# Kernel tuning notes

Measured on AMD Instinct MI355X. Metric: run time of the kernel, lower is better.

Reference implementation:

```python
import jax, jax.numpy as jnp
import numpy as np

N_EVENT = 100000
N_TRACE = 20000
E_EE = 1000000
E_ET = 500000
E_TE = 500000
D = 128          # embedding_dim == hidden_dim
OUT = 64         # output_dim
L = 3            # num_layers
NTYPES_EDGES = 3 # edge types
B = 64           # graphs per batch


def setup_inputs() -> dict:
    key = jax.random.key(0)
    ks = jax.random.split(key, 16)
    s = 1.0 / np.sqrt(D)
    inp = {
        "event_ids": jnp.arange(N_EVENT, dtype=jnp.int64 if jax.config.jax_enable_x64 else jnp.int32),
        "trace_ids": jnp.arange(N_TRACE, dtype=jnp.int64 if jax.config.jax_enable_x64 else jnp.int32),
        "e2e_src": jax.random.randint(ks[0], (E_EE,), 0, N_EVENT),
        "e2e_dst": jax.random.randint(ks[1], (E_EE,), 0, N_EVENT),
        "e2t_src": jax.random.randint(ks[2], (E_ET,), 0, N_EVENT),
        "e2t_dst": jax.random.randint(ks[3], (E_ET,), 0, N_TRACE),
        "t2e_src": jax.random.randint(ks[4], (E_TE,), 0, N_TRACE),
        "t2e_dst": jax.random.randint(ks[5], (E_TE,), 0, N_EVENT),
        "event_batch": jnp.sort(jax.random.randint(ks[6], (N_EVENT,), 0, B)),
        "trace_batch": jnp.sort(jax.random.randint(ks[7], (N_TRACE,), 0, B)),
        # learned parameters
        "emb_event": jax.random.normal(ks[8], (N_EVENT, D), jnp.float32),
        "emb_trace": jax.random.normal(ks[9], (N_TRACE, D), jnp.float32),
        # per-layer, per-edge-type SAGEConv weights: lin_l (neighbor, with bias), lin_r (root, no bias)
        "Wl": jax.random.normal(ks[10], (L, NTYPES_EDGES, D, D), jnp.float32) * s,
        "bl": jnp.zeros((L, NTYPES_EDGES, D), jnp.float32),
        "Wr": jax.random.normal(ks[11], (L, NTYPES_EDGES, D, D), jnp.float32) * s,
        # output MLP head
        "W1": jax.random.normal(ks[12], (D, D), jnp.float32) * s,
        "b1": jnp.zeros((D,), jnp.float32),
        "W2": jax.random.normal(ks[13], (OUT, D), jnp.float32) * s,
        "b2": jnp.zeros((OUT,), jnp.float32),
    }
    return inp


def reference(event_ids, trace_ids, e2e_src, e2e_dst, e2t_src, e2t_dst,
              t2e_src, t2e_dst, event_batch, trace_batch,
              emb_event, emb_trace, Wl, bl, Wr, W1, b1, W2, b2):
    def seg_mean(x_src, src, dst, n_dst):
        # mean-aggregate source features onto destination nodes (SAGEConv default aggr)
        s = jax.ops.segment_sum(x_src[src], dst, num_segments=n_dst)
        c = jax.ops.segment_sum(jnp.ones(dst.shape, x_src.dtype), dst, num_segments=n_dst)
        return s / jnp.maximum(c, 1.0)[:, None]

    # per-node-type embedding lookup
    x = {"event": emb_event[event_ids], "trace": emb_trace[trace_ids]}
    n = {"event": event_ids.shape[0], "trace": trace_ids.shape[0]}
    # edge types: (src_type, dst_type, src_idx, dst_idx), conv index matches Wl/bl/Wr axis 1
    edges = [
        ("event", "event", e2e_src, e2e_dst),
        ("event", "trace", e2t_src, e2t_dst),
        ("trace", "event", t2e_src, t2e_dst),
    ]
    n_layers = Wl.shape[0]
    for l in range(n_layers):
        new = {k: jnp.zeros((n[k], Wl.shape[-2]), x[k].dtype) for k in x}
        for i, (st, dt, s_idx, d_idx) in enumerate(edges):
            m = seg_mean(x[st], s_idx, d_idx, n[dt])
            # SAGEConv: lin_l(mean neighbors) + lin_r(root); HeteroConv aggr='sum' across edge types
            new[dt] = new[dt] + m @ Wl[l, i].T + bl[l, i] + x[dt] @ Wr[l, i].T
        x = new
    # global_add_pool per node type, then stack+sum over node types
    pooled = (jax.ops.segment_sum(x["event"], event_batch, num_segments=B)
              + jax.ops.segment_sum(x["trace"], trace_batch, num_segments=B))
    h = jax.nn.relu(pooled @ W1.T + b1)
    return h @ W2.T + b2
```

## Files before the change

### kernel.cpp

```cpp
#include <hip/hip_runtime.h>
#include <hip/hip_bf16.h>


#define D 128
#define NB 64
#define OUTD 64
#define NLAY 3

typedef __bf16 bf16;
typedef __bf16 bf16x4 __attribute__((ext_vector_type(4)));
typedef __bf16 bf16x8 __attribute__((ext_vector_type(8)));
typedef float  f32x16 __attribute__((ext_vector_type(16)));

#define LOAD16_TO_LDS(gp, lp) \
    __builtin_amdgcn_global_load_lds((const __attribute__((address_space(1))) void*)(gp), \
                                     (__attribute__((address_space(3))) void*)(lp), 16, 0, 0)

__global__ void gather_all(const float* __restrict__ embE, const int* __restrict__ idsE,
                           bf16* __restrict__ xE, int nE,
                           const float* __restrict__ embT, const int* __restrict__ idsT,
                           bf16* __restrict__ xT, int nT) {
    int idx = blockIdx.x * blockDim.x + threadIdx.x;
    const float* emb; const int* ids; bf16* x;
    int tE = nE * 32;
    if (idx < tE) { emb = embE; ids = idsE; x = xE; }
    else {
        idx -= tE;
        if (idx >= nT * 32) return;
        emb = embT; ids = idsT; x = xT;
    }
    int r = idx >> 5, v = idx & 31;
    float4 f = ((const float4*)(emb + (size_t)ids[r] * D))[v];
    bf16x4 o;
    o[0] = (bf16)f.x; o[1] = (bf16)f.y; o[2] = (bf16)f.z; o[3] = (bf16)f.w;
    ((bf16x4*)(x + (size_t)r * D))[v] = o;
}

__global__ void hist_all(const int* __restrict__ dEE, const int* __restrict__ dET,
                         const int* __restrict__ dTE, int nEE, int nET, int nTE,
                         int* __restrict__ degEE, int* __restrict__ degET, int* __restrict__ degTE,
                         int* __restrict__ rkEE, int* __restrict__ rkET, int* __restrict__ rkTE) {
    int e = blockIdx.x * blockDim.x + threadIdx.x;
    const int* dst; int* deg; int* rk;
    if (e < nEE) { dst = dEE; deg = degEE; rk = rkEE; }
    else {
        e -= nEE;
        if (e < nET) { dst = dET; deg = degET; rk = rkET; }
        else {
            e -= nET;
            if (e >= nTE) return;
            dst = dTE; deg = degTE; rk = rkTE;
        }
    }
    rk[e] = atomicAdd(&deg[dst[e]], 1);
}

__global__ void scan_p1_all(const int* __restrict__ dA, int* __restrict__ oA, int* __restrict__ sA, int nA,
                            const int* __restrict__ dB, int* __restrict__ oB, int* __restrict__ sB, int nB,
                            const int* __restrict__ dC, int* __restrict__ oC, int* __restrict__ sC, int nC) {
    int nbA = (nA + 1023) >> 10, nbB = (nB + 1023) >> 10;
    int b = blockIdx.x;
    const int* deg; int* off; int* bsum; int n; int lb;
    if (b < nbA) { deg = dA; off = oA; bsum = sA; n = nA; lb = b; }
    else if (b < nbA + nbB) { deg = dB; off = oB; bsum = sB; n = nB; lb = b - nbA; }
    else { deg = dC; off = oC; bsum = sC; n = nC; lb = b - nbA - nbB; }
    __shared__ int s[256];
    int t = threadIdx.x;
    int base = lb * 1024 + t * 4;
    int v[4];
    #pragma unroll
    for (int i = 0; i < 4; ++i) v[i] = (base + i < n) ? deg[base + i] : 0;
    int tot = v[0] + v[1] + v[2] + v[3];
    s[t] = tot;
    __syncthreads();
    for (int st = 1; st < 256; st <<= 1) {
        int x = (t >= st) ? s[t - st] : 0;
        __syncthreads();
        s[t] += x;
        __syncthreads();
    }
    int run = s[t] - tot;
    #pragma unroll
    for (int i = 0; i < 4; ++i) {
        if (base + i < n) off[base + i] = run;
        run += v[i];
    }
    if (t == 255) bsum[lb] = s[255];
}

__global__ void scan_p2_all(int* __restrict__ sA, int nbA,
                            int* __restrict__ sB, int nbB,
                            int* __restrict__ sC, int nbC) {
    int* bsum; int nb;
    if (blockIdx.x == 0) { bsum = sA; nb = nbA; }
    else if (blockIdx.x == 1) { bsum = sB; nb = nbB; }
    else { bsum = sC; nb = nbC; }
    __shared__ int s[256];
    int t = threadIdx.x;
    int v = (t < nb) ? bsum[t] : 0;
    s[t] = v;
    __syncthreads();
    for (int st = 1; st < 256; st <<= 1) {
        int x = (t >= st) ? s[t - st] : 0;
        __syncthreads();
        s[t] += x;
        __syncthreads();
    }
    if (t < nb) bsum[t] = s[t] - v;
    if (t == 0) bsum[nb] = s[255];
}

__global__ void scan_p3_all(int* __restrict__ oA, const int* __restrict__ sA, int nA,
                            int* __restrict__ oB, const int* __restrict__ sB, int nB,
                            int* __restrict__ oC, const int* __restrict__ sC, int nC) {
    int cbA = (nA + 255) >> 8, cbB = (nB + 255) >> 8;
    int b = blockIdx.x;
    int* off; const int* bsum; int n; int lb;
    if (b < cbA) { off = oA; bsum = sA; n = nA; lb = b; }
    else if (b < cbA + cbB) { off = oB; bsum = sB; n = nB; lb = b - cbA; }
    else { off = oC; bsum = sC; n = nC; lb = b - cbA - cbB; }
    int i = lb * 256 + threadIdx.x;
    if (i < n) off[i] += bsum[i >> 10];
    if (i == 0) off[n] = bsum[(n + 1023) >> 10];
}

__global__ void adj_fill_all(const int* __restrict__ sEE, const int* __restrict__ dEE, int nEE,
                             const int* __restrict__ sET, const int* __restrict__ dET, int nET,
                             const int* __restrict__ sTE, const int* __restrict__ dTE, int nTE,
                             const int* __restrict__ oEE, const int* __restrict__ oET,
                             const int* __restrict__ oTE,
                             const int* __restrict__ rkEE, const int* __restrict__ rkET,
                             const int* __restrict__ rkTE,
                             int* __restrict__ adjEE, int* __restrict__ adjET,
                             int* __restrict__ adjTE) {
    int e = blockIdx.x * blockDim.x + threadIdx.x;
    const int* src; const int* dst; const int* off; const int* rk; int* adj;
    if (e < nEE) { src = sEE; dst = dEE; off = oEE; rk = rkEE; adj = adjEE; }
    else {
        e -= nEE;
        if (e < nET) { src = sET; dst = dET; off = oET; rk = rkET; adj = adjET; }
        else {
            e -= nET;
            if (e >= nTE) return;
            src = sTE; dst = dTE; off = oTE; rk = rkTE; adj = adjTE;
        }
    }
    adj[off[dst[e]] + rk[e]] = src[e];
}

__global__ void agg_all(const bf16* __restrict__ xE, const bf16* __restrict__ xT,
                        const int* __restrict__ offEE, const int* __restrict__ adjEE,
                        const int* __restrict__ offTE, const int* __restrict__ adjTE,
                        const int* __restrict__ offET, const int* __restrict__ adjET,
                        bf16* __restrict__ mEE, bf16* __restrict__ mTE, bf16* __restrict__ mET,
                        int nE, int nT) {
    int gw = (blockIdx.x * blockDim.x + threadIdx.x) >> 6;
    int lane = threadIdx.x & 63;
    int qE = (nE + 3) >> 2, qT = (nT + 3) >> 2;
    const bf16* xsrc; const int* off; const int* adj; bf16* out; int ndst;
    if (gw < qE) { xsrc = xE; off = offEE; adj = adjEE; out = mEE; ndst = nE; }
    else if (gw < 2 * qE) { gw -= qE; xsrc = xT; off = offTE; adj = adjTE; out = mTE; ndst = nE; }
    else {
        gw -= 2 * qE;
        if (gw >= qT) return;
        xsrc = xE; off = offET; adj = adjET; out = mET; ndst = nT;
    }
    int sub = lane >> 4;
    int sl  = lane & 15;
    int row = gw * 4 + sub;
    if (row >= ndst) row = ndst - 1;
    int s0 = off[row], s1 = off[row + 1];
    float a[8] = {};
    int j = s0;
    for (; j + 8 <= s1; j += 8) {
        int ii[8];
        #pragma unroll
        for (int u = 0; u < 8; ++u) ii[u] = adj[j + u];
        bf16x8 v[8];
        #pragma unroll
        for (int u = 0; u < 8; ++u) v[u] = ((const bf16x8*)(xsrc + (size_t)ii[u] * D))[sl];
        #pragma unroll
        for (int u = 0; u < 8; ++u)
            #pragma unroll
            for (int e = 0; e < 8; ++e) a[e] += (float)v[u][e];
    }
    for (; j + 4 <= s1; j += 4) {
        int i0 = adj[j], i1 = adj[j + 1], i2 = adj[j + 2], i3 = adj[j + 3];
        bf16x8 v0 = ((const bf16x8*)(xsrc + (size_t)i0 * D))[sl];
        bf16x8 v1 = ((const bf16x8*)(xsrc + (size_t)i1 * D))[sl];
        bf16x8 v2 = ((const bf16x8*)(xsrc + (size_t)i2 * D))[sl];
        bf16x8 v3 = ((const bf16x8*)(xsrc + (size_t)i3 * D))[sl];
        #pragma unroll
        for (int e = 0; e < 8; ++e)
            a[e] += (float)v0[e] + (float)v1[e] + (float)v2[e] + (float)v3[e];
    }
    for (; j < s1; ++j) {
        int i0 = adj[j];
        bf16x8 v0 = ((const bf16x8*)(xsrc + (size_t)i0 * D))[sl];
        #pragma unroll
        for (int e = 0; e < 8; ++e) a[e] += (float)v0[e];
    }
    float inv = 1.0f / fmaxf((float)(s1 - s0), 1.0f);
    bf16x8 o;
    #pragma unroll
    for (int e = 0; e < 8; ++e) o[e] = (bf16)(a[e] * inv);
    ((bf16x8*)(out + (size_t)row * D))[sl] = o;
}

__global__ void prep_weights_packed(const float* __restrict__ Wl, const float* __restrict__ Wr,
                                    bf16* __restrict__ wbuf) {
    int idx = blockIdx.x * blockDim.x + threadIdx.x;
    if (idx >= NLAY * 5 * 2048) return;
    int l = idx / (5 * 2048);
    int rem = idx - l * 5 * 2048;
    int mat = rem >> 11;
    int q = rem & 2047;
    int lane = q & 63, t = (q >> 6) & 7, w = q >> 9;
    int r = w * 32 + (lane & 31);
    int c = t * 16 + (lane >> 5) * 8;
    size_t l3 = (size_t)l * 3;
    const float* s0;
    const float* s1 = nullptr;
    switch (mat) {
        case 0: s0 = Wl + (l3 + 0) * D * D; break;
        case 1: s0 = Wl + (l3 + 2) * D * D; break;
        case 2: s0 = Wr + (l3 + 0) * D * D; s1 = Wr + (l3 + 2) * D * D; break;
        case 3: s0 = Wl + (l3 + 1) * D * D; break;
        default: s0 = Wr + (l3 + 1) * D * D; break;
    }
    bf16x8 hi, lo;
    #pragma unroll
    for (int e = 0; e < 8; ++e) {
        float v = s0[r * D + c + e];
        if (s1) v += s1[r * D + c + e];
        bf16 h = (bf16)v;
        hi[e] = h;
        lo[e] = (bf16)(v - (float)h);
    }
    bf16* base = wbuf + (size_t)l * 10 * D * D;
    ((bf16x8*)(base + (size_t)(2 * mat) * D * D))[q] = hi;
    ((bf16x8*)(base + (size_t)(2 * mat + 1) * D * D))[q] = lo;
}

__global__ void prep_bias(const float* __restrict__ bl, float* __restrict__ bbuf) {
    int idx = blockIdx.x * blockDim.x + threadIdx.x;
    if (idx >= NLAY * D) return;
    int l = idx >> 7, o = idx & (D - 1);
    bbuf[l * 2 * D + o]     = bl[(size_t)(l * 3 + 0) * D + o] + bl[(size_t)(l * 3 + 2) * D + o];
    bbuf[l * 2 * D + D + o] = bl[(size_t)(l * 3 + 1) * D + o];
}

__device__ __forceinline__ void gemm_body(const bf16* A0, const bf16* A1, const bf16* A2,
                                          const bf16* Wp, const float* bias, bf16* out,
                                          int M, int nm, int row0, bf16* As) {
    int tid = threadIdx.x;
    int wave = tid >> 6, lane = tid & 63;
    int m = lane & 31, half = lane >> 5;

    f32x16 acc[4];
    #pragma unroll
    for (int rt = 0; rt < 4; ++rt)
        #pragma unroll
        for (int i = 0; i < 16; ++i) acc[rt][i] = 0.f;

    const bf16* Aptr[3] = {A0, A1, A2};
    #pragma unroll
    for (int s = 0; s < 3; ++s) {
        if (s >= nm) break;
        if (s) __syncthreads();
        const bf16* wph = Wp + (size_t)(2 * s) * D * D + ((size_t)wave * 512 + lane) * 8;
        const bf16* wpl = wph + D * D;
        bf16x8 bh[8], blo[8];
        #pragma unroll
        for (int t = 0; t < 8; ++t) {
            bh[t]  = *(const bf16x8*)(wph + t * 512);
            blo[t] = *(const bf16x8*)(wpl + t * 512);
        }
        const bf16* Amat = Aptr[s];
        #pragma unroll
        for (int p = 0; p < 8; ++p) {
            int si = p * 256 + tid;
            int r = si >> 4, u = si & 15;
            int gr = row0 + r; if (gr >= M) gr = M - 1;
            int gc = (u ^ (r & 15)) * 8;
            LOAD16_TO_LDS(Amat + (size_t)gr * D + gc, As + (size_t)(p * 4 + wave) * 512);
        }
        __syncthreads();

        #pragma unroll
        for (int t = 0; t < 8; ++t) {
            bf16x8 af[4];
            #pragma unroll
            for (int rt = 0; rt < 4; ++rt) {
                int r = rt * 32 + m;
                int c = t * 2 + half;
                af[rt] = *(const bf16x8*)(As + ((size_t)r * 16 + (c ^ (r & 15))) * 8);
            }
            #pragma unroll
            for (int rt = 0; rt < 4; ++rt)
                acc[rt] = __builtin_amdgcn_mfma_f32_32x32x16_bf16(af[rt], bh[t], acc[rt], 0, 0, 0);
            #pragma unroll
            for (int rt = 0; rt < 4; ++rt)
                acc[rt] = __builtin_amdgcn_mfma_f32_32x32x16_bf16(af[rt], blo[t], acc[rt], 0, 0, 0);
        }
    }

    int col = wave * 32 + m;
    float bv = bias[col];
    #pragma unroll
    for (int rt = 0; rt < 4; ++rt) {
        #pragma unroll
        for (int r = 0; r < 16; ++r) {
            int row = row0 + rt * 32 + (r & 3) + 8 * (r >> 2) + 4 * half;
            if (row < M) out[(size_t)row * D + col] = (bf16)(acc[rt][r] + bv);
        }
    }
}

__global__ __launch_bounds__(256) void gemm_all(const bf16* __restrict__ eA0, const bf16* __restrict__ eA1,
                                                const bf16* __restrict__ eA2, const bf16* __restrict__ eW,
                                                const float* __restrict__ eB, bf16* __restrict__ eOut,
                                                int Me, int bE,
                                                const bf16* __restrict__ tA0, const bf16* __restrict__ tA1,
                                                const bf16* __restrict__ tW, const float* __restrict__ tB,
                                                bf16* __restrict__ tOut, int Mt) {
    __shared__ bf16 As[128 * 128];
    if ((int)blockIdx.x < bE)
        gemm_body(eA0, eA1, eA2, eW, eB, eOut, Me, 3, blockIdx.x * 128, As);
    else
        gemm_body(tA0, tA1, (const bf16*)nullptr, tW, tB, tOut, Mt, 2, (blockIdx.x - bE) * 128, As);
}

__global__ void pool_all(const bf16* __restrict__ xE, const int* __restrict__ bEv, int nE, int pbE,
                         const bf16* __restrict__ xT, const int* __restrict__ bTr, int nT,
                         float* __restrict__ pooled) {
    int c = threadIdx.x;
    int blk = blockIdx.x;
    const bf16* x; const int* batch; int n, r0;
    if (blk < pbE) { x = xE; batch = bEv; n = nE; r0 = blk * 64; }
    else { x = xT; batch = bTr; n = nT; r0 = (blk - pbE) * 64; }
    int r1 = min(r0 + 64, n);
    if (r0 >= r1) return;
    int cur = batch[r0];
    float acc = 0.f;
    for (int r = r0; r < r1; ++r) {
        int b = batch[r];
        if (b != cur) { atomicAdd(&pooled[cur * D + c], acc); acc = 0.f; cur = b; }
        acc += (float)x[(size_t)r * D + c];
    }
    atomicAdd(&pooled[cur * D + c], acc);
}

__global__ void head_kernel(const float* __restrict__ pooled, const float* __restrict__ W1,
                            const float* __restrict__ b1, const float* __restrict__ W2,
                            const float* __restrict__ b2, float* __restrict__ out) {
    __shared__ float p[D];
    __shared__ float h[D];
    int b = blockIdx.x, t = threadIdx.x;
    p[t] = pooled[b * D + t];
    __syncthreads();
    float s = b1[t];
    const float* w = W1 + (size_t)t * D;
    #pragma unroll 4
    for (int k = 0; k < D; ++k) s += p[k] * w[k];
    h[t] = fmaxf(s, 0.f);
    __syncthreads();
    if (t < OUTD) {
        float s2 = b2[t];
        const float* w2 = W2 + (size_t)t * D;
        #pragma unroll 4
        for (int k = 0; k < D; ++k) s2 += h[k] * w2[k];
        out[b * OUTD + t] = s2;
    }
}

extern "C" void kernel_launch(void* const* d_in, const int* in_sizes, int n_in,
                              void* d_out, int out_size, void* d_ws, size_t ws_size,
                              hipStream_t stream) {
    const int* event_ids   = (const int*)d_in[0];
    const int* trace_ids   = (const int*)d_in[1];
    const int* e2e_src     = (const int*)d_in[2];
    const int* e2e_dst     = (const int*)d_in[3];
    const int* e2t_src     = (const int*)d_in[4];
    const int* e2t_dst     = (const int*)d_in[5];
    const int* t2e_src     = (const int*)d_in[6];
    const int* t2e_dst     = (const int*)d_in[7];
    const int* event_batch = (const int*)d_in[8];
    const int* trace_batch = (const int*)d_in[9];
    const float* emb_event = (const float*)d_in[10];
    const float* emb_trace = (const float*)d_in[11];
    const float* Wl        = (const float*)d_in[12];
    const float* bl        = (const float*)d_in[13];
    const float* Wr        = (const float*)d_in[14];
    const float* W1        = (const float*)d_in[15];
    const float* b1        = (const float*)d_in[16];
    const float* W2        = (const float*)d_in[17];
    const float* b2        = (const float*)d_in[18];

    const int NE = in_sizes[0];
    const int NT = in_sizes[1];
    const int EE = in_sizes[2];
    const int ET = in_sizes[4];
    const int TE = in_sizes[6];

    size_t cur = 0;
    auto alloc = [&](size_t bytes) -> void* {
        cur = (cur + 255) & ~(size_t)255;
        void* p = (char*)d_ws + cur;
        cur += bytes;
        return p;
    };
    bf16* x_event   = (bf16*)alloc((size_t)NE * D * 2);
    bf16* x_trace   = (bf16*)alloc((size_t)NT * D * 2);
    bf16* nx_event  = (bf16*)alloc((size_t)NE * D * 2);
    bf16* nx_trace  = (bf16*)alloc((size_t)NT * D * 2);
    bf16* m_ee      = (bf16*)alloc((size_t)NE * D * 2);
    bf16* m_te      = (bf16*)alloc((size_t)NE * D * 2);
    bf16* m_et      = (bf16*)alloc((size_t)NT * D * 2);
    float* pooled   = (float*)alloc((size_t)NB * D * 4);
    bf16* wbuf      = (bf16*)alloc((size_t)NLAY * 10 * D * D * 2);
    float* bbuf     = (float*)alloc((size_t)NLAY * 2 * D * 4);
    int* zbase  = (int*)alloc(((size_t)NE + NT + NE) * 4);
    int* deg_ee = zbase;
    int* deg_et = deg_ee + NE;
    int* deg_te = deg_et + NT;
    int* off_ee = (int*)alloc((size_t)(NE + 1) * 4);
    int* adj_ee = (int*)alloc((size_t)EE * 4);
    int* off_et = (int*)alloc((size_t)(NT + 1) * 4);
    int* adj_et = (int*)alloc((size_t)ET * 4);
    int* off_te = (int*)alloc((size_t)(NE + 1) * 4);
    int* adj_te = (int*)alloc((size_t)TE * 4);
    int* bsum_ee = (int*)alloc(((size_t)(NE + 1023) / 1024 + 1) * 4);
    int* bsum_et = (int*)alloc(((size_t)(NT + 1023) / 1024 + 1) * 4);
    int* bsum_te = (int*)alloc(((size_t)(NE + 1023) / 1024 + 1) * 4);
    int* rk_ee = (int*)m_ee;
    int* rk_et = (int*)m_te;
    int* rk_te = (int*)m_et;
    (void)ws_size; (void)n_in; (void)out_size;

    const int nbE = (NE + 1023) / 1024;
    const int nbT = (NT + 1023) / 1024;

    hipMemsetAsync(zbase, 0, ((size_t)NE + NT + NE) * 4, stream);

    gather_all<<<((NE + NT) * 32 + 255) / 256, 256, 0, stream>>>(
        emb_event, event_ids, x_event, NE, emb_trace, trace_ids, x_trace, NT);

    prep_weights_packed<<<(NLAY * 5 * 2048 + 255) / 256, 256, 0, stream>>>(Wl, Wr, wbuf);
    prep_bias<<<(NLAY * D + 255) / 256, 256, 0, stream>>>(bl, bbuf);

    hist_all<<<(EE + ET + TE + 255) / 256, 256, 0, stream>>>(
        e2e_dst, e2t_dst, t2e_dst, EE, ET, TE,
        deg_ee, deg_et, deg_te, rk_ee, rk_et, rk_te);
    scan_p1_all<<<nbE + nbT + nbE, 256, 0, stream>>>(
        deg_ee, off_ee, bsum_ee, NE, deg_et, off_et, bsum_et, NT, deg_te, off_te, bsum_te, NE);
    scan_p2_all<<<3, 256, 0, stream>>>(bsum_ee, nbE, bsum_et, nbT, bsum_te, nbE);
    scan_p3_all<<<((NE + 255) >> 8) * 2 + ((NT + 255) >> 8), 256, 0, stream>>>(
        off_ee, bsum_ee, NE, off_et, bsum_et, NT, off_te, bsum_te, NE);
    adj_fill_all<<<(EE + ET + TE + 255) / 256, 256, 0, stream>>>(
        e2e_src, e2e_dst, EE, e2t_src, e2t_dst, ET, t2e_src, t2e_dst, TE,
        off_ee, off_et, off_te, rk_ee, rk_et, rk_te, adj_ee, adj_et, adj_te);

    const int qE = (NE + 3) >> 2, qT = (NT + 3) >> 2;
    const int aggBlocks = (2 * qE + qT + 3) / 4;
    const int bE = (NE + 127) / 128, bT = (NT + 127) / 128;
    for (int l = 0; l < NLAY; ++l) {
        const bf16* wl_ev = wbuf + (size_t)l * 10 * D * D;
        const bf16* wl_tr = wl_ev + (size_t)6 * D * D;
        const float* be = bbuf + (size_t)l * 2 * D;
        const float* bt = be + D;

        agg_all<<<aggBlocks, 256, 0, stream>>>(x_event, x_trace,
                                               off_ee, adj_ee, off_te, adj_te, off_et, adj_et,
                                               m_ee, m_te, m_et, NE, NT);
        gemm_all<<<bE + bT, 256, 0, stream>>>(m_ee, m_te, x_event, wl_ev, be, nx_event, NE, bE,
                                              m_et, x_trace, wl_tr, bt, nx_trace, NT);

        bf16* t;
        t = x_event; x_event = nx_event; nx_event = t;
        t = x_trace; x_trace = nx_trace; nx_trace = t;
    }

    hipMemsetAsync(pooled, 0, (size_t)NB * D * 4, stream);
    const int pbE = (NE + 63) / 64, pbT = (NT + 63) / 64;
    pool_all<<<pbE + pbT, D, 0, stream>>>(x_event, event_batch, NE, pbE,
                                          x_trace, trace_batch, NT, pooled);

    head_kernel<<<NB, D, 0, stream>>>(pooled, W1, b1, W2, b2, (float*)d_out);
}
```

Measured before the change: 681.3 us.

## Fuse neighbor mean aggregation into GEMM tile load and merge setup kernels

Measured after the change: 736.4 us. 1.08x slower.

```diff
diff --git a/kernel.cpp b/kernel.cpp
--- a/kernel.cpp
+++ b/kernel.cpp
@@ -16,11 +16,11 @@
     __builtin_amdgcn_global_load_lds((const __attribute__((address_space(1))) void*)(gp), \
                                      (__attribute__((address_space(3))) void*)(lp), 16, 0, 0)
 
-__global__ void gather_all(const float* __restrict__ embE, const int* __restrict__ idsE,
-                           bf16* __restrict__ xE, int nE,
-                           const float* __restrict__ embT, const int* __restrict__ idsT,
-                           bf16* __restrict__ xT, int nT) {
-    int idx = blockIdx.x * blockDim.x + threadIdx.x;
+
+__device__ __forceinline__ void gather_dev(int vb, const float* embE, const int* idsE,
+                                           bf16* xE, int nE, const float* embT,
+                                           const int* idsT, bf16* xT, int nT) {
+    int idx = vb * 256 + threadIdx.x;
     const float* emb; const int* ids; bf16* x;
     int tE = nE * 32;
     if (idx < tE) { emb = embE; ids = idsE; x = xE; }
@@ -36,11 +36,11 @@
     ((bf16x4*)(x + (size_t)r * D))[v] = o;
 }
 
-__global__ void hist_all(const int* __restrict__ dEE, const int* __restrict__ dET,
-                         const int* __restrict__ dTE, int nEE, int nET, int nTE,
-                         int* __restrict__ degEE, int* __restrict__ degET, int* __restrict__ degTE,
-                         int* __restrict__ rkEE, int* __restrict__ rkET, int* __restrict__ rkTE) {
-    int e = blockIdx.x * blockDim.x + threadIdx.x;
+__device__ __forceinline__ void hist_dev(int vb, const int* dEE, const int* dET,
+                                         const int* dTE, int nEE, int nET, int nTE,
+                                         int* degEE, int* degET, int* degTE,
+                                         int* rkEE, int* rkET, int* rkTE) {
+    int e = vb * 256 + threadIdx.x;
     const int* dst; int* deg; int* rk;
     if (e < nEE) { dst = dEE; deg = degEE; rk = rkEE; }
     else {
@@ -53,6 +53,80 @@
         }
     }
     rk[e] = atomicAdd(&deg[dst[e]], 1);
+}
+
+__device__ __forceinline__ void prepw_dev(int vb, const float* Wl, const float* Wr,
+                                          bf16* wbuf) {
+    int idx = vb * 256 + threadIdx.x;
+    if (idx >= NLAY * 5 * 2048) return;
+    int l = idx / (5 * 2048);
+    int rem = idx - l * 5 * 2048;
+    int mat = rem >> 11;
+    int q = rem & 2047;
+    int lane = q & 63, t = (q >> 6) & 7, w = q >> 9;
+    int r = w * 32 + (lane & 31);
+    int c = t * 16 + (lane >> 5) * 8;
+    size_t l3 = (size_t)l * 3;
+    const float* s0;
+    const float* s1 = nullptr;
+    switch (mat) {
+        case 0: s0 = Wl + (l3 + 0) * D * D; break;
+        case 1: s0 = Wl + (l3 + 2) * D * D; break;
+        case 2: s0 = Wr + (l3 + 0) * D * D; s1 = Wr + (l3 + 2) * D * D; break;
+        case 3: s0 = Wl + (l3 + 1) * D * D; break;
+        default: s0 = Wr + (l3 + 1) * D * D; break;
+    }
+    bf16x8 hi, lo;
+    #pragma unroll
+    for (int e = 0; e < 8; ++e) {
+        float v = s0[r * D + c + e];
+        if (s1) v += s1[r * D + c + e];
+        bf16 h = (bf16)v;
+        hi[e] = h;
+        lo[e] = (bf16)(v - (float)h);
+    }
+    bf16* base = wbuf + (size_t)l * 10 * D * D;
+    ((bf16x8*)(base + (size_t)(2 * mat) * D * D))[q] = hi;
+    ((bf16x8*)(base + (size_t)(2 * mat + 1) * D * D))[q] = lo;
+}
+
+__device__ __forceinline__ void prepb_dev(int vb, const float* bl, float* bbuf) {
+    int idx = vb * 256 + threadIdx.x;
+    if (idx >= NLAY * D) return;
+    int l = idx >> 7, o = idx & (D - 1);
+    bbuf[l * 2 * D + o]     = bl[(size_t)(l * 3 + 0) * D + o] + bl[(size_t)(l * 3 + 2) * D + o];
+    bbuf[l * 2 * D + D + o] = bl[(size_t)(l * 3 + 1) * D + o];
+}
+
+__global__ void front_all(const float* __restrict__ embE, const int* __restrict__ idsE,
+                          bf16* __restrict__ xE, int nE,
+                          const float* __restrict__ embT, const int* __restrict__ idsT,
+                          bf16* __restrict__ xT, int nT,
+                          const int* __restrict__ dEE, const int* __restrict__ dET,
+                          const int* __restrict__ dTE, int nEE, int nET, int nTE,
+                          int* __restrict__ degEE, int* __restrict__ degET,
+                          int* __restrict__ degTE,
+                          int* __restrict__ rkEE, int* __restrict__ rkET,
+                          int* __restrict__ rkTE,
+                          const float* __restrict__ Wl, const float* __restrict__ Wr,
+                          const float* __restrict__ bl,
+                          bf16* __restrict__ wbuf, float* __restrict__ bbuf,
+                          int nHist, int nGather) {
+    int b = blockIdx.x;
+    int trip = nHist * 3;
+    if (b < trip) {
+        int g = b / 3, r = b - g * 3;
+        if (r == 2) hist_dev(g, dEE, dET, dTE, nEE, nET, nTE,
+                             degEE, degET, degTE, rkEE, rkET, rkTE);
+        else {
+            int gb = g * 2 + r;
+            if (gb < nGather) gather_dev(gb, embE, idsE, xE, nE, embT, idsT, xT, nT);
+        }
+    } else {
+        int pb = b - trip;
+        if (pb < 120) prepw_dev(pb, Wl, Wr, wbuf);
+        else prepb_dev(pb - 120, bl, bbuf);
+    }
 }
 
 __global__ void scan_p1_all(const int* __restrict__ dA, int* __restrict__ oA, int* __restrict__ sA, int nA,
@@ -148,111 +222,11 @@
     adj[off[dst[e]] + rk[e]] = src[e];
 }
 
-__global__ void agg_all(const bf16* __restrict__ xE, const bf16* __restrict__ xT,
-                        const int* __restrict__ offEE, const int* __restrict__ adjEE,
-                        const int* __restrict__ offTE, const int* __restrict__ adjTE,
-                        const int* __restrict__ offET, const int* __restrict__ adjET,
-                        bf16* __restrict__ mEE, bf16* __restrict__ mTE, bf16* __restrict__ mET,
-                        int nE, int nT) {
-    int gw = (blockIdx.x * blockDim.x + threadIdx.x) >> 6;
-    int lane = threadIdx.x & 63;
-    int qE = (nE + 3) >> 2, qT = (nT + 3) >> 2;
-    const bf16* xsrc; const int* off; const int* adj; bf16* out; int ndst;
-    if (gw < qE) { xsrc = xE; off = offEE; adj = adjEE; out = mEE; ndst = nE; }
-    else if (gw < 2 * qE) { gw -= qE; xsrc = xT; off = offTE; adj = adjTE; out = mTE; ndst = nE; }
-    else {
-        gw -= 2 * qE;
-        if (gw >= qT) return;
-        xsrc = xE; off = offET; adj = adjET; out = mET; ndst = nT;
-    }
-    int sub = lane >> 4;
-    int sl  = lane & 15;
-    int row = gw * 4 + sub;
-    if (row >= ndst) row = ndst - 1;
-    int s0 = off[row], s1 = off[row + 1];
-    float a[8] = {};
-    int j = s0;
-    for (; j + 8 <= s1; j += 8) {
-        int ii[8];
-        #pragma unroll
-        for (int u = 0; u < 8; ++u) ii[u] = adj[j + u];
-        bf16x8 v[8];
-        #pragma unroll
-        for (int u = 0; u < 8; ++u) v[u] = ((const bf16x8*)(xsrc + (size_t)ii[u] * D))[sl];
-        #pragma unroll
-        for (int u = 0; u < 8; ++u)
-            #pragma unroll
-            for (int e = 0; e < 8; ++e) a[e] += (float)v[u][e];
-    }
-    for (; j + 4 <= s1; j += 4) {
-        int i0 = adj[j], i1 = adj[j + 1], i2 = adj[j + 2], i3 = adj[j + 3];
-        bf16x8 v0 = ((const bf16x8*)(xsrc + (size_t)i0 * D))[sl];
-        bf16x8 v1 = ((const bf16x8*)(xsrc + (size_t)i1 * D))[sl];
-        bf16x8 v2 = ((const bf16x8*)(xsrc + (size_t)i2 * D))[sl];
-        bf16x8 v3 = ((const bf16x8*)(xsrc + (size_t)i3 * D))[sl];
-        #pragma unroll
-        for (int e = 0; e < 8; ++e)
-            a[e] += (float)v0[e] + (float)v1[e] + (float)v2[e] + (float)v3[e];
-    }
-    for (; j < s1; ++j) {
-        int i0 = adj[j];
-        bf16x8 v0 = ((const bf16x8*)(xsrc + (size_t)i0 * D))[sl];
-        #pragma unroll
-        for (int e = 0; e < 8; ++e) a[e] += (float)v0[e];
-    }
-    float inv = 1.0f / fmaxf((float)(s1 - s0), 1.0f);
-    bf16x8 o;
-    #pragma unroll
-    for (int e = 0; e < 8; ++e) o[e] = (bf16)(a[e] * inv);
-    ((bf16x8*)(out + (size_t)row * D))[sl] = o;
-}
-
-__global__ void prep_weights_packed(const float* __restrict__ Wl, const float* __restrict__ Wr,
-                                    bf16* __restrict__ wbuf) {
-    int idx = blockIdx.x * blockDim.x + threadIdx.x;
-    if (idx >= NLAY * 5 * 2048) return;
-    int l = idx / (5 * 2048);
-    int rem = idx - l * 5 * 2048;
-    int mat = rem >> 11;
-    int q = rem & 2047;
-    int lane = q & 63, t = (q >> 6) & 7, w = q >> 9;
-    int r = w * 32 + (lane & 31);
-    int c = t * 16 + (lane >> 5) * 8;
-    size_t l3 = (size_t)l * 3;
-    const float* s0;
-    const float* s1 = nullptr;
-    switch (mat) {
-        case 0: s0 = Wl + (l3 + 0) * D * D; break;
-        case 1: s0 = Wl + (l3 + 2) * D * D; break;
-        case 2: s0 = Wr + (l3 + 0) * D * D; s1 = Wr + (l3 + 2) * D * D; break;
-        case 3: s0 = Wl + (l3 + 1) * D * D; break;
-        default: s0 = Wr + (l3 + 1) * D * D; break;
-    }
-    bf16x8 hi, lo;
-    #pragma unroll
-    for (int e = 0; e < 8; ++e) {
-        float v = s0[r * D + c + e];
-        if (s1) v += s1[r * D + c + e];
-        bf16 h = (bf16)v;
-        hi[e] = h;
-        lo[e] = (bf16)(v - (float)h);
-    }
-    bf16* base = wbuf + (size_t)l * 10 * D * D;
-    ((bf16x8*)(base + (size_t)(2 * mat) * D * D))[q] = hi;
-    ((bf16x8*)(base + (size_t)(2 * mat + 1) * D * D))[q] = lo;
-}
-
-__global__ void prep_bias(const float* __restrict__ bl, float* __restrict__ bbuf) {
-    int idx = blockIdx.x * blockDim.x + threadIdx.x;
-    if (idx >= NLAY * D) return;
-    int l = idx >> 7, o = idx & (D - 1);
-    bbuf[l * 2 * D + o]     = bl[(size_t)(l * 3 + 0) * D + o] + bl[(size_t)(l * 3 + 2) * D + o];
-    bbuf[l * 2 * D + D + o] = bl[(size_t)(l * 3 + 1) * D + o];
-}
-
-__device__ __forceinline__ void gemm_body(const bf16* A0, const bf16* A1, const bf16* A2,
-                                          const bf16* Wp, const float* bias, bf16* out,
-                                          int M, int nm, int row0, bf16* As) {
+__device__ __forceinline__ void gemm_body(const bf16* x0, const int* off0, const int* adj0,
+                                          const bf16* x1, const int* off1, const int* adj1,
+                                          const bf16* x2, const int* off2, const int* adj2,
+                                          int nm, const bf16* Wp, const float* bias,
+                                          bf16* out, int M, int row0, bf16* As) {
     int tid = threadIdx.x;
     int wave = tid >> 6, lane = tid & 63;
     int m = lane & 31, half = lane >> 5;
@@ -263,11 +237,75 @@
         #pragma unroll
         for (int i = 0; i < 16; ++i) acc[rt][i] = 0.f;
 
-    const bf16* Aptr[3] = {A0, A1, A2};
+    const bf16* xs[3]  = {x0, x1, x2};
+    const int* offs[3] = {off0, off1, off2};
+    const int* adjs[3] = {adj0, adj1, adj2};
+
     #pragma unroll
     for (int s = 0; s < 3; ++s) {
         if (s >= nm) break;
         if (s) __syncthreads();
+
+        if (adjs[s]) {
+            const bf16* xsrc = xs[s];
+            const int* off = offs[s];
+            const int* adj = adjs[s];
+            int sub = lane >> 4;
+            int sl  = lane & 15;
+            #pragma unroll
+            for (int g = 0; g < 8; ++g) {
+                int r = wave * 32 + g * 4 + sub;
+                int gr = row0 + r; if (gr >= M) gr = M - 1;
+                int s0 = off[gr], s1 = off[gr + 1];
+                float a[8] = {};
+                int j = s0;
+                for (; j + 8 <= s1; j += 8) {
+                    int ii[8];
+                    #pragma unroll
+                    for (int u = 0; u < 8; ++u) ii[u] = adj[j + u];
+                    bf16x8 v[8];
+                    #pragma unroll
+                    for (int u = 0; u < 8; ++u)
+                        v[u] = ((const bf16x8*)(xsrc + (size_t)ii[u] * D))[sl];
+                    #pragma unroll
+                    for (int u = 0; u < 8; ++u)
+                        #pragma unroll
+                        for (int e = 0; e < 8; ++e) a[e] += (float)v[u][e];
+                }
+                for (; j + 4 <= s1; j += 4) {
+                    int i0 = adj[j], i1 = adj[j + 1], i2 = adj[j + 2], i3 = adj[j + 3];
+                    bf16x8 v0 = ((const bf16x8*)(xsrc + (size_t)i0 * D))[sl];
+                    bf16x8 v1 = ((const bf16x8*)(xsrc + (size_t)i1 * D))[sl];
+                    bf16x8 v2 = ((const bf16x8*)(xsrc + (size_t)i2 * D))[sl];
+                    bf16x8 v3 = ((const bf16x8*)(xsrc + (size_t)i3 * D))[sl];
+                    #pragma unroll
+                    for (int e = 0; e < 8; ++e)
+                        a[e] += (float)v0[e] + (float)v1[e] + (float)v2[e] + (float)v3[e];
+                }
+                for (; j < s1; ++j) {
+                    int i0 = adj[j];
+                    bf16x8 v0 = ((const bf16x8*)(xsrc + (size_t)i0 * D))[sl];
+                    #pragma unroll
+                    for (int e = 0; e < 8; ++e) a[e] += (float)v0[e];
+                }
+                float inv = 1.0f / fmaxf((float)(s1 - s0), 1.0f);
+                bf16x8 o;
+                #pragma unroll
+                for (int e = 0; e < 8; ++e) o[e] = (bf16)(a[e] * inv);
+                ((bf16x8*)As)[r * 16 + (sl ^ (r & 15))] = o;
+            }
+        } else {
+            const bf16* Amat = xs[s];
+            #pragma unroll
+            for (int p = 0; p < 8; ++p) {
+                int si = p * 256 + tid;
+                int r = si >> 4, u = si & 15;
+                int gr = row0 + r; if (gr >= M) gr = M - 1;
+                int gc = (u ^ (r & 15)) * 8;
+                LOAD16_TO_LDS(Amat + (size_t)gr * D + gc, As + (size_t)(p * 4 + wave) * 512);
+            }
+        }
+
         const bf16* wph = Wp + (size_t)(2 * s) * D * D + ((size_t)wave * 512 + lane) * 8;
         const bf16* wpl = wph + D * D;
         bf16x8 bh[8], blo[8];
@@ -275,15 +313,6 @@
         for (int t = 0; t < 8; ++t) {
             bh[t]  = *(const bf16x8*)(wph + t * 512);
             blo[t] = *(const bf16x8*)(wpl + t * 512);
-        }
-        const bf16* Amat = Aptr[s];
-        #pragma unroll
-        for (int p = 0; p < 8; ++p) {
-            int si = p * 256 + tid;
-            int r = si >> 4, u = si & 15;
-            int gr = row0 + r; if (gr >= M) gr = M - 1;
-            int gc = (u ^ (r & 15)) * 8;
-            LOAD16_TO_LDS(Amat + (size_t)gr * D + gc, As + (size_t)(p * 4 + wave) * 512);
         }
         __syncthreads();
 
@@ -317,18 +346,26 @@
     }
 }
 
-__global__ __launch_bounds__(256) void gemm_all(const bf16* __restrict__ eA0, const bf16* __restrict__ eA1,
-                                                const bf16* __restrict__ eA2, const bf16* __restrict__ eW,
-                                                const float* __restrict__ eB, bf16* __restrict__ eOut,
-                                                int Me, int bE,
-                                                const bf16* __restrict__ tA0, const bf16* __restrict__ tA1,
+__global__ __launch_bounds__(256) void gemm_all(const bf16* __restrict__ xE,
+                                                const bf16* __restrict__ xT,
+                                                const int* __restrict__ offEE, const int* __restrict__ adjEE,
+                                                const int* __restrict__ offTE, const int* __restrict__ adjTE,
+                                                const int* __restrict__ offET, const int* __restrict__ adjET,
+                                                const bf16* __restrict__ eW, const float* __restrict__ eB,
+                                                bf16* __restrict__ eOut, int Me, int bE,
                                                 const bf16* __restrict__ tW, const float* __restrict__ tB,
                                                 bf16* __restrict__ tOut, int Mt) {
     __shared__ bf16 As[128 * 128];
     if ((int)blockIdx.x < bE)
-        gemm_body(eA0, eA1, eA2, eW, eB, eOut, Me, 3, blockIdx.x * 128, As);
+        gemm_body(xE, offEE, adjEE,
+                  xT, offTE, adjTE,
+                  xE, nullptr, nullptr,
+                  3, eW, eB, eOut, Me, blockIdx.x * 128, As);
     else
-        gemm_body(tA0, tA1, (const bf16*)nullptr, tW, tB, tOut, Mt, 2, (blockIdx.x - bE) * 128, As);
+        gemm_body(xE, offET, adjET,
+                  xT, nullptr, nullptr,
+                  nullptr, nullptr, nullptr,
+                  2, tW, tB, tOut, Mt, ((int)blockIdx.x - bE) * 128, As);
 }
 
 __global__ void pool_all(const bf16* __restrict__ xE, const int* __restrict__ bEv, int nE, int pbE,
@@ -414,9 +451,6 @@
     bf16* x_trace   = (bf16*)alloc((size_t)NT * D * 2);
     bf16* nx_event  = (bf16*)alloc((size_t)NE * D * 2);
     bf16* nx_trace  = (bf16*)alloc((size_t)NT * D * 2);
-    bf16* m_ee      = (bf16*)alloc((size_t)NE * D * 2);
-    bf16* m_te      = (bf16*)alloc((size_t)NE * D * 2);
-    bf16* m_et      = (bf16*)alloc((size_t)NT * D * 2);
     float* pooled   = (float*)alloc((size_t)NB * D * 4);
     bf16* wbuf      = (bf16*)alloc((size_t)NLAY * 10 * D * D * 2);
     float* bbuf     = (float*)alloc((size_t)NLAY * 2 * D * 4);
@@ -433,9 +467,9 @@
     int* bsum_ee = (int*)alloc(((size_t)(NE + 1023) / 1024 + 1) * 4);
     int* bsum_et = (int*)alloc(((size_t)(NT + 1023) / 1024 + 1) * 4);
     int* bsum_te = (int*)alloc(((size_t)(NE + 1023) / 1024 + 1) * 4);
-    int* rk_ee = (int*)m_ee;
-    int* rk_et = (int*)m_te;
-    int* rk_te = (int*)m_et;
+    int* rk_ee = (int*)nx_event;
+    int* rk_et = ((int*)nx_event) + EE;
+    int* rk_te = (int*)nx_trace;
     (void)ws_size; (void)n_in; (void)out_size;
 
     const int nbE = (NE + 1023) / 1024;
@@ -443,15 +477,14 @@
 
     hipMemsetAsync(zbase, 0, ((size_t)NE + NT + NE) * 4, stream);
 
-    gather_all<<<((NE + NT) * 32 + 255) / 256, 256, 0, stream>>>(
-        emb_event, event_ids, x_event, NE, emb_trace, trace_ids, x_trace, NT);
-
-    prep_weights_packed<<<(NLAY * 5 * 2048 + 255) / 256, 256, 0, stream>>>(Wl, Wr, wbuf);
-    prep_bias<<<(NLAY * D + 255) / 256, 256, 0, stream>>>(bl, bbuf);
-
-    hist_all<<<(EE + ET + TE + 255) / 256, 256, 0, stream>>>(
+    const int nGather = ((NE + NT) * 32 + 255) / 256;
+    const int nHist = (EE + ET + TE + 255) / 256;
+    front_all<<<3 * nHist + 122, 256, 0, stream>>>(
+        emb_event, event_ids, x_event, NE, emb_trace, trace_ids, x_trace, NT,
         e2e_dst, e2t_dst, t2e_dst, EE, ET, TE,
-        deg_ee, deg_et, deg_te, rk_ee, rk_et, rk_te);
+        deg_ee, deg_et, deg_te, rk_ee, rk_et, rk_te,
+        Wl, Wr, bl, wbuf, bbuf, nHist, nGather);
+
     scan_p1_all<<<nbE + nbT + nbE, 256, 0, stream>>>(
         deg_ee, off_ee, bsum_ee, NE, deg_et, off_et, bsum_et, NT, deg_te, off_te, bsum_te, NE);
     scan_p2_all<<<3, 256, 0, stream>>>(bsum_ee, nbE, bsum_et, nbT, bsum_te, nbE);
@@ -461,8 +494,6 @@
         e2e_src, e2e_dst, EE, e2t_src, e2t_dst, ET, t2e_src, t2e_dst, TE,
         off_ee, off_et, off_te, rk_ee, rk_et, rk_te, adj_ee, adj_et, adj_te);
 
-    const int qE = (NE + 3) >> 2, qT = (NT + 3) >> 2;
-    const int aggBlocks = (2 * qE + qT + 3) / 4;
     const int bE = (NE + 127) / 128, bT = (NT + 127) / 128;
     for (int l = 0; l < NLAY; ++l) {
         const bf16* wl_ev = wbuf + (size_t)l * 10 * D * D;
@@ -470,11 +501,10 @@
         const float* be = bbuf + (size_t)l * 2 * D;
         const float* bt = be + D;
 
-        agg_all<<<aggBlocks, 256, 0, stream>>>(x_event, x_trace,
-                                               off_ee, adj_ee, off_te, adj_te, off_et, adj_et,
-                                               m_ee, m_te, m_et, NE, NT);
-        gemm_all<<<bE + bT, 256, 0, stream>>>(m_ee, m_te, x_event, wl_ev, be, nx_event, NE, bE,
-                                              m_et, x_trace, wl_tr, bt, nx_trace, NT);
+        gemm_all<<<bE + bT, 256, 0, stream>>>(x_event, x_trace,
+                                              off_ee, adj_ee, off_te, adj_te, off_et, adj_et,
+                                              wl_ev, be, nx_event, NE, bE,
+                                              wl_tr, bt, nx_trace, NT);
 
         bf16* t;
         t = x_event; x_event = nx_event; nx_event = t;
```
